# Kernel tuning notes

Hardware: AMD Instinct MI355X
Metric: run time of the kernel (lower is better)

## Reference

```python
import jax, jax.numpy as jnp
import numpy as np

B, S, E = 2, 2048, 1024
H = 16
D = E // H  # head_dim = 64
SCALE = D ** -0.5


def _rope_cos_sin(seq_len, dim, dtype=jnp.float32):
    inv_freq = 1.0 / (10000.0 ** (jnp.arange(0, dim, 2, dtype=jnp.float32) / dim))
    pos = jnp.arange(seq_len, dtype=jnp.float32)
    freqs = pos[:, None] * inv_freq[None, :]  # [S, D/2]
    return jnp.cos(freqs).astype(dtype), jnp.sin(freqs).astype(dtype)


def _apply_rope(x, cos, sin):
    # x: [B, H, S, D]; interleaved complex rotation on (even, odd) pairs
    x2 = x.reshape(*x.shape[:-1], D // 2, 2)
    xr, xi = x2[..., 0], x2[..., 1]
    c = cos[None, None, :, :]
    s = sin[None, None, :, :]
    out_r = xr * c - xi * s
    out_i = xr * s + xi * c
    return jnp.stack([out_r, out_i], axis=-1).reshape(x.shape)


def setup_inputs() -> dict:
    key = jax.random.key(0)
    k1, k2, k3, k4, k5 = jax.random.split(key, 5)
    query = jax.random.normal(k1, (B, S, E), dtype=jnp.float32)
    key_t = jax.random.normal(k2, (B, S, E), dtype=jnp.float32)
    value = jax.random.normal(k3, (B, S, E), dtype=jnp.float32)
    w_qkv = jax.random.normal(k4, (3 * E, E), dtype=jnp.float32) * 0.02
    w_out = jax.random.normal(k5, (E, E), dtype=jnp.float32) * 0.02
    return {"query": query, "key": key_t, "value": value,
            "w_qkv": w_qkv, "w_out": w_out}


def reference(query, key, value, w_qkv, w_out):
    # Fused QKV projection from query only (matches original module)
    qkv = jnp.einsum('bse,fe->bsf', query, w_qkv)  # [B, S, 3E]
    q, k, v = jnp.split(qkv, 3, axis=-1)
    to_heads = lambda t: t.reshape(B, S, H, D).transpose(0, 2, 1, 3)  # [B,H,S,D]
    q, k, v = to_heads(q), to_heads(k), to_heads(v)

    cos, sin = _rope_cos_sin(S, D, q.dtype)
    q = _apply_rope(q, cos, sin)
    k = _apply_rope(k, cos, sin)

    # Standard scaled dot-product attention (eval mode, no mask, no dropout)
    attn = jnp.einsum('bhsd,bhtd->bhst', q, k) * SCALE
    attn = jax.nn.softmax(attn.astype(jnp.float32), axis=-1).astype(q.dtype)
    ctx = jnp.einsum('bhst,bhtd->bhsd', attn, v)  # [B,H,S,D]

    out = ctx.transpose(0, 2, 1, 3).reshape(B, S, E)
    return jnp.einsum('bse,fe->bsf', out, w_out)
```

## Files before the change

### kernel.cpp

```cpp
#include <hip/hip_runtime.h>
#include <math.h>

typedef __attribute__((ext_vector_type(8))) __bf16 bf16x8;
typedef __attribute__((ext_vector_type(4))) __bf16 bf16x4;
typedef __attribute__((ext_vector_type(4))) float f32x4;

constexpr int kBATCH = 2;
constexpr int kS = 2048;
constexpr int kE = 1024;
constexpr int kH = 16;
constexpr int kD = 64;
constexpr float kScale = 0.125f;

__device__ inline void gl2lds16(const void* g, void* l) {
    __builtin_amdgcn_global_load_lds((const __attribute__((address_space(1))) void*)g,
                                     (__attribute__((address_space(3))) void*)l, 16, 0, 0);
}

__global__ __launch_bounds__(256) void cvt2_kernel(const float* __restrict__ a, __bf16* __restrict__ oa, int na,
                                                   const float* __restrict__ b, __bf16* __restrict__ ob) {
    int idx = (blockIdx.x * 256 + threadIdx.x) * 4;
    const float* src;
    __bf16* dst;
    if (idx < na) { src = a + idx; dst = oa + idx; }
    else          { src = b + (idx - na); dst = ob + (idx - na); }
    float4 f = *(const float4*)src;
    bf16x4 r;
    r[0] = (__bf16)f.x; r[1] = (__bf16)f.y; r[2] = (__bf16)f.z; r[3] = (__bf16)f.w;
    *(bf16x4*)dst = r;
}

template <int TN, typename TC>
__global__ __launch_bounds__(256) void gemm_bt_kernel(const __bf16* __restrict__ A,
                                                      const __bf16* __restrict__ W,
                                                      TC* __restrict__ C,
                                                      int M, int N, int K) {
    constexpr int NI = TN / 32;
    __shared__ __bf16 As[128 * 64] __attribute__((aligned(16)));
    __shared__ __bf16 Bs[TN * 64] __attribute__((aligned(16)));

    const int tid  = threadIdx.x;
    const int lane = tid & 63;
    const int quad = lane >> 4;
    const int l16  = lane & 15;
    const int rx   = l16 & 7;
    const int wave = tid >> 6;
    const int wm   = (wave >> 1) * 64;
    const int wn   = (wave & 1) * (TN / 2);
    const int m0   = blockIdx.y * 128;
    const int n0   = blockIdx.x * TN;

    const int srow8  = lane >> 3;
    const int schunk = ((lane & 7) ^ srow8) * 8;

    f32x4 zero = {0.f, 0.f, 0.f, 0.f};
    f32x4 acc[4][NI];
#pragma unroll
    for (int i = 0; i < 4; ++i)
#pragma unroll
        for (int j = 0; j < NI; ++j) acc[i][j] = zero;

    for (int kt = 0; kt < K; kt += 64) {
        __syncthreads();
#pragma unroll
        for (int i = 0; i < 4; ++i) {
            int rbase = wave * 32 + i * 8;
            gl2lds16(A + (size_t)(m0 + rbase + srow8) * K + kt + schunk, &As[rbase * 64]);
        }
#pragma unroll
        for (int i = 0; i < NI; ++i) {
            int rbase = wave * (TN / 4) + i * 8;
            gl2lds16(W + (size_t)(n0 + rbase + srow8) * K + kt + schunk, &Bs[rbase * 64]);
        }
        __syncthreads();

#pragma unroll
        for (int kk = 0; kk < 2; ++kk) {
            bf16x8 af[4], bf[NI];
#pragma unroll
            for (int mi = 0; mi < 4; ++mi)
                af[mi] = *(const bf16x8*)(&As[(wm + mi * 16 + l16) * 64 + (((kk * 4 + quad) ^ rx)) * 8]);
#pragma unroll
            for (int ni = 0; ni < NI; ++ni)
                bf[ni] = *(const bf16x8*)(&Bs[(wn + ni * 16 + l16) * 64 + (((kk * 4 + quad) ^ rx)) * 8]);
#pragma unroll
            for (int mi = 0; mi < 4; ++mi)
#pragma unroll
                for (int ni = 0; ni < NI; ++ni)
                    acc[mi][ni] = __builtin_amdgcn_mfma_f32_16x16x32_bf16(af[mi], bf[ni], acc[mi][ni], 0, 0, 0);
        }
    }

#pragma unroll
    for (int mi = 0; mi < 4; ++mi)
#pragma unroll
        for (int ni = 0; ni < NI; ++ni)
#pragma unroll
            for (int r = 0; r < 4; ++r) {
                int row = m0 + wm + mi * 16 + quad * 4 + r;
                int col = n0 + wn + ni * 16 + l16;
                C[(size_t)row * N + col] = (TC)acc[mi][ni][r];
            }
}

__global__ __launch_bounds__(256) void rope_vtrans_kernel(const __bf16* __restrict__ qkv,
                                                          __bf16* __restrict__ qd,
                                                          __bf16* __restrict__ kd,
                                                          __bf16* __restrict__ vt) {
    __shared__ __bf16 tile[64 * 72] __attribute__((aligned(16)));

    if (blockIdx.x < 8192) {
        int tid = blockIdx.x * 256 + threadIdx.x;
        int i = tid & 31;
        int h = (tid >> 5) & (kH - 1);
        int s = (tid >> 9) & (kS - 1);
        int b = tid >> 20;

        size_t rowbase = (size_t)(b * kS + s) * (3 * kE);
        int coff = h * kD + 2 * i;

        float qr = (float)qkv[rowbase + coff];
        float qi = (float)qkv[rowbase + coff + 1];
        float kr = (float)qkv[rowbase + kE + coff];
        float ki = (float)qkv[rowbase + kE + coff + 1];

        float inv = expf(-(float)i * (9.210340371976184f / 32.0f));
        float ang = (float)s * inv;
        float cv = cosf(ang);
        float sv = sinf(ang);

        size_t qbase = ((size_t)(b * kH + h) * kS + s) * kD + 2 * i;
        qd[qbase]     = (__bf16)(kScale * (qr * cv - qi * sv));
        qd[qbase + 1] = (__bf16)(kScale * (qr * sv + qi * cv));
        kd[qbase]     = (__bf16)(kr * cv - ki * sv);
        kd[qbase + 1] = (__bf16)(kr * sv + ki * cv);
    } else {
        int flat = blockIdx.x - 8192;
        int s0 = (flat & 31) * 64;
        int bh = flat >> 5;
        int b = bh >> 4, h = bh & 15;
        int tid = threadIdx.x;

#pragma unroll
        for (int p = 0; p < 2; ++p) {
            int c = tid + p * 256;
            int r = c >> 3, jc = c & 7;
            *(bf16x8*)&tile[r * 72 + jc * 8] =
                *(const bf16x8*)(qkv + (size_t)(b * kS + s0 + r) * (3 * kE) + 2 * kE + h * kD + jc * 8);
        }
        __syncthreads();
#pragma unroll
        for (int p = 0; p < 2; ++p) {
            int c = tid + p * 256;
            int d = c >> 3, jt = c & 7;
            bf16x8 v;
#pragma unroll
            for (int u = 0; u < 8; ++u) {
                int src = (jt >> 2) * 32 + ((u >> 2) << 4) + ((jt & 3) << 2) + (u & 3);
                v[u] = tile[src * 72 + d];
            }
            *(bf16x8*)(vt + (size_t)(bh * kD + d) * kS + s0 + jt * 8) = v;
        }
    }
}

__global__ __launch_bounds__(128) void attn_kernel(const __bf16* __restrict__ qd,
                                                   const __bf16* __restrict__ kd,
                                                   const __bf16* __restrict__ vt,
                                                   __bf16* __restrict__ ctx,
                                                   const float* __restrict__ wout,
                                                   __bf16* __restrict__ woutb) {
    __shared__ __bf16 Ks[2][64 * 64] __attribute__((aligned(16)));
    __shared__ __bf16 Vs[2][64 * 64] __attribute__((aligned(16)));

    const int lane = threadIdx.x & 63;
    const int wave = threadIdx.x >> 6;
    const int quad = lane >> 4;
    const int l16  = lane & 15;
    const int rx   = l16 & 7;

    {
        int base = blockIdx.x * 1024 + threadIdx.x * 8;
        float4 f0 = *(const float4*)(wout + base);
        float4 f1 = *(const float4*)(wout + base + 4);
        bf16x8 r;
        r[0] = (__bf16)f0.x; r[1] = (__bf16)f0.y; r[2] = (__bf16)f0.z; r[3] = (__bf16)f0.w;
        r[4] = (__bf16)f1.x; r[5] = (__bf16)f1.y; r[6] = (__bf16)f1.z; r[7] = (__bf16)f1.w;
        *(bf16x8*)(woutb + base) = r;
    }

    const int flat = blockIdx.x;
    const int s    = flat >> 3;
    const int bh   = (flat & 7) * 4 + (s >> 5);
    const int q0   = (s & 31) * 64;
    const int b  = bh >> 4;
    const int h  = bh & 15;

    const __bf16* qp = qd + (size_t)bh * kS * kD;
    const __bf16* kp = kd + (size_t)bh * kS * kD;
    const __bf16* vp = vt + (size_t)bh * kD * kS;

    const int srow8  = lane >> 3;
    const int schunk = ((lane & 7) ^ srow8) * 8;

    bf16x8 aq[2][2];
#pragma unroll
    for (int mi = 0; mi < 2; ++mi) {
        const __bf16* qrow = qp + (size_t)(q0 + wave * 32 + mi * 16 + l16) * kD + quad * 8;
        aq[mi][0] = *(const bf16x8*)(qrow);
        aq[mi][1] = *(const bf16x8*)(qrow + 32);
    }

    bf16x8 vone;
#pragma unroll
    for (int u = 0; u < 8; ++u) vone[u] = (__bf16)1.0f;

    f32x4 zero = {0.f, 0.f, 0.f, 0.f};
    f32x4 acc[2][4];
    f32x4 asum[2];
#pragma unroll
    for (int mi = 0; mi < 2; ++mi) {
        asum[mi] = zero;
#pragma unroll
        for (int i = 0; i < 4; ++i) acc[mi][i] = zero;
    }

#pragma unroll
    for (int c = 0; c < 4; ++c) {
        int i = wave * 4 + c;
        gl2lds16(kp + (size_t)(i * 8 + srow8) * kD + schunk, &Ks[0][i * 512]);
        gl2lds16(vp + (size_t)(i * 8 + srow8) * kS + schunk, &Vs[0][i * 512]);
    }

    const int nT = kS / 64;
    for (int it = 0; it < nT; ++it) {
        const int buf = it & 1;
        __syncthreads();
        if (it + 1 < nT) {
            int t1 = (it + 1) * 64;
#pragma unroll
            for (int c = 0; c < 4; ++c) {
                int i = wave * 4 + c;
                gl2lds16(kp + (size_t)(t1 + i * 8 + srow8) * kD + schunk, &Ks[buf ^ 1][i * 512]);
                gl2lds16(vp + (size_t)(i * 8 + srow8) * kS + t1 + schunk, &Vs[buf ^ 1][i * 512]);
            }
        }

#pragma unroll
        for (int ks = 0; ks < 2; ++ks) {
            bf16x8 ak[2][2];
#pragma unroll
            for (int t2 = 0; t2 < 2; ++t2) {
                int krow = (ks * 2 + t2) * 16 + l16;
                ak[t2][0] = *(const bf16x8*)&Ks[buf][krow * 64 + ((quad      ^ rx)) * 8];
                ak[t2][1] = *(const bf16x8*)&Ks[buf][krow * 64 + (((quad + 4) ^ rx)) * 8];
            }
            bf16x8 ap[2];
#pragma unroll
            for (int mi = 0; mi < 2; ++mi) {
                f32x4 s0 = __builtin_amdgcn_mfma_f32_16x16x32_bf16(ak[0][0], aq[mi][0], zero, 0, 0, 0);
                s0 = __builtin_amdgcn_mfma_f32_16x16x32_bf16(ak[0][1], aq[mi][1], s0, 0, 0, 0);
                f32x4 s1 = __builtin_amdgcn_mfma_f32_16x16x32_bf16(ak[1][0], aq[mi][0], zero, 0, 0, 0);
                s1 = __builtin_amdgcn_mfma_f32_16x16x32_bf16(ak[1][1], aq[mi][1], s1, 0, 0, 0);
                bf16x8 p;
                p[0] = (__bf16)__expf(s0[0]); p[1] = (__bf16)__expf(s0[1]);
                p[2] = (__bf16)__expf(s0[2]); p[3] = (__bf16)__expf(s0[3]);
                p[4] = (__bf16)__expf(s1[0]); p[5] = (__bf16)__expf(s1[1]);
                p[6] = (__bf16)__expf(s1[2]); p[7] = (__bf16)__expf(s1[3]);
                ap[mi] = p;
            }
#pragma unroll
            for (int mi = 0; mi < 2; ++mi)
                asum[mi] = __builtin_amdgcn_mfma_f32_16x16x32_bf16(ap[mi], vone, asum[mi], 0, 0, 0);
#pragma unroll
            for (int nt = 0; nt < 4; ++nt) {
                int drow = nt * 16 + l16;
                bf16x8 bv = *(const bf16x8*)&Vs[buf][drow * 64 + (((ks * 4 + quad) ^ rx)) * 8];
                acc[0][nt] = __builtin_amdgcn_mfma_f32_16x16x32_bf16(ap[0], bv, acc[0][nt], 0, 0, 0);
                acc[1][nt] = __builtin_amdgcn_mfma_f32_16x16x32_bf16(ap[1], bv, acc[1][nt], 0, 0, 0);
            }
        }
    }

#pragma unroll
    for (int mi = 0; mi < 2; ++mi)
#pragma unroll
        for (int r = 0; r < 4; ++r) {
            float inv_l = 1.0f / asum[mi][r];
            int srow_q = q0 + wave * 32 + mi * 16 + quad * 4 + r;
#pragma unroll
            for (int nt = 0; nt < 4; ++nt) {
                int col = h * kD + nt * 16 + l16;
                ctx[(size_t)(b * kS + srow_q) * kE + col] = (__bf16)(acc[mi][nt][r] * inv_l);
            }
        }
}

extern "C" void kernel_launch(void* const* d_in, const int* in_sizes, int n_in,
                              void* d_out, int out_size, void* d_ws, size_t ws_size,
                              hipStream_t stream) {
    const float* query = (const float*)d_in[0];
    const float* w_qkv = (const float*)d_in[3];
    const float* w_out = (const float*)d_in[4];
    float* out = (float*)d_out;

    const int M = kBATCH * kS;
    const int nQ = M * kE;
    const int nWqkv = 3 * kE * kE;

    char* ws = (char*)d_ws;
    __bf16* qkv_raw = (__bf16*)ws;
    __bf16* ctx     = (__bf16*)ws;
    __bf16* w_out_b = (__bf16*)(ws + (size_t)8388608);
    __bf16* qd      = (__bf16*)(ws + (size_t)25165824);
    __bf16* kd      = (__bf16*)(ws + (size_t)33554432);
    __bf16* vt      = (__bf16*)(ws + (size_t)41943040);
    __bf16* query_b = qd;
    __bf16* w_qkv_b = kd;

    cvt2_kernel<<<(nQ + nWqkv) / 1024, 256, 0, stream>>>(query, query_b, nQ, w_qkv, w_qkv_b);

    gemm_bt_kernel<128, __bf16>
        <<<dim3(3 * kE / 128, M / 128), 256, 0, stream>>>(query_b, w_qkv_b, qkv_raw, M, 3 * kE, kE);

    rope_vtrans_kernel<<<8192 + 1024, 256, 0, stream>>>(qkv_raw, qd, kd, vt);

    attn_kernel<<<1024, 128, 0, stream>>>(qd, kd, vt, ctx, w_out, w_out_b);

    gemm_bt_kernel<64, float>
        <<<dim3(kE / 64, M / 128), 256, 0, stream>>>(ctx, w_out_b, out, M, kE, kE);
}
```

Measured before the change: 226.7 us.

## Split attention KV range across waves and read K/V directly from global

Each block now runs four waves: two query halves times two key halves, each wave covering half the sequence. Partial sums and row sums are combined through shared memory at the end. The LDS double-buffered staging of K and V tiles is removed, so each wave loads its MFMA fragments straight from global memory and relies on the caches. This adds waves per block for more latency hiding, but loses LDS reuse and issues many small, strided global loads.

New measurement: 278.5 us. +22.8%, slower.

```diff
diff --git a/kernel.cpp b/kernel.cpp
--- a/kernel.cpp
+++ b/kernel.cpp
@@ -164,29 +164,27 @@
     }
 }
 
-__global__ __launch_bounds__(128) void attn_kernel(const __bf16* __restrict__ qd,
-                                                   const __bf16* __restrict__ kd,
-                                                   const __bf16* __restrict__ vt,
-                                                   __bf16* __restrict__ ctx,
-                                                   const float* __restrict__ wout,
-                                                   __bf16* __restrict__ woutb) {
-    __shared__ __bf16 Ks[2][64 * 64] __attribute__((aligned(16)));
-    __shared__ __bf16 Vs[2][64 * 64] __attribute__((aligned(16)));
-
-    const int lane = threadIdx.x & 63;
-    const int wave = threadIdx.x >> 6;
-    const int quad = lane >> 4;
-    const int l16  = lane & 15;
-    const int rx   = l16 & 7;
+__global__ __launch_bounds__(256, 4) void attn_kernel(const __bf16* __restrict__ qd,
+                                                      const __bf16* __restrict__ kd,
+                                                      const __bf16* __restrict__ vt,
+                                                      __bf16* __restrict__ ctx,
+                                                      const float* __restrict__ wout,
+                                                      __bf16* __restrict__ woutb) {
+    __shared__ float comb[2][64][40];
+
+    const int lane  = threadIdx.x & 63;
+    const int wave  = threadIdx.x >> 6;
+    const int qhalf = wave >> 1;
+    const int khalf = wave & 1;
+    const int quad  = lane >> 4;
+    const int l16   = lane & 15;
 
     {
-        int base = blockIdx.x * 1024 + threadIdx.x * 8;
-        float4 f0 = *(const float4*)(wout + base);
-        float4 f1 = *(const float4*)(wout + base + 4);
-        bf16x8 r;
-        r[0] = (__bf16)f0.x; r[1] = (__bf16)f0.y; r[2] = (__bf16)f0.z; r[3] = (__bf16)f0.w;
-        r[4] = (__bf16)f1.x; r[5] = (__bf16)f1.y; r[6] = (__bf16)f1.z; r[7] = (__bf16)f1.w;
-        *(bf16x8*)(woutb + base) = r;
+        int base = blockIdx.x * 1024 + threadIdx.x * 4;
+        float4 f = *(const float4*)(wout + base);
+        bf16x4 r;
+        r[0] = (__bf16)f.x; r[1] = (__bf16)f.y; r[2] = (__bf16)f.z; r[3] = (__bf16)f.w;
+        *(bf16x4*)(woutb + base) = r;
     }
 
     const int flat = blockIdx.x;
@@ -200,13 +198,10 @@
     const __bf16* kp = kd + (size_t)bh * kS * kD;
     const __bf16* vp = vt + (size_t)bh * kD * kS;
 
-    const int srow8  = lane >> 3;
-    const int schunk = ((lane & 7) ^ srow8) * 8;
-
     bf16x8 aq[2][2];
 #pragma unroll
     for (int mi = 0; mi < 2; ++mi) {
-        const __bf16* qrow = qp + (size_t)(q0 + wave * 32 + mi * 16 + l16) * kD + quad * 8;
+        const __bf16* qrow = qp + (size_t)(q0 + qhalf * 32 + mi * 16 + l16) * kD + quad * 8;
         aq[mi][0] = *(const bf16x8*)(qrow);
         aq[mi][1] = *(const bf16x8*)(qrow + 32);
     }
@@ -225,43 +220,27 @@
         for (int i = 0; i < 4; ++i) acc[mi][i] = zero;
     }
 
-#pragma unroll
-    for (int c = 0; c < 4; ++c) {
-        int i = wave * 4 + c;
-        gl2lds16(kp + (size_t)(i * 8 + srow8) * kD + schunk, &Ks[0][i * 512]);
-        gl2lds16(vp + (size_t)(i * 8 + srow8) * kS + schunk, &Vs[0][i * 512]);
-    }
-
-    const int nT = kS / 64;
-    for (int it = 0; it < nT; ++it) {
-        const int buf = it & 1;
-        __syncthreads();
-        if (it + 1 < nT) {
-            int t1 = (it + 1) * 64;
-#pragma unroll
-            for (int c = 0; c < 4; ++c) {
-                int i = wave * 4 + c;
-                gl2lds16(kp + (size_t)(t1 + i * 8 + srow8) * kD + schunk, &Ks[buf ^ 1][i * 512]);
-                gl2lds16(vp + (size_t)(i * 8 + srow8) * kS + t1 + schunk, &Vs[buf ^ 1][i * 512]);
-            }
-        }
-
+    const __bf16* kfrag = kp + (size_t)(khalf * 1024 + l16) * kD + quad * 8;
+    const __bf16* vfrag = vp + (size_t)l16 * kS + khalf * 1024 + quad * 8;
+
+#pragma unroll 2
+    for (int it = 0; it < 16; ++it) {
+        const __bf16* kt = kfrag + it * (64 * kD);
+        const __bf16* vtile = vfrag + it * 64;
 #pragma unroll
         for (int ks = 0; ks < 2; ++ks) {
-            bf16x8 ak[2][2];
-#pragma unroll
-            for (int t2 = 0; t2 < 2; ++t2) {
-                int krow = (ks * 2 + t2) * 16 + l16;
-                ak[t2][0] = *(const bf16x8*)&Ks[buf][krow * 64 + ((quad      ^ rx)) * 8];
-                ak[t2][1] = *(const bf16x8*)&Ks[buf][krow * 64 + (((quad + 4) ^ rx)) * 8];
-            }
+            const __bf16* kk = kt + ks * (32 * kD);
+            bf16x8 ak00 = *(const bf16x8*)(kk);
+            bf16x8 ak01 = *(const bf16x8*)(kk + 32);
+            bf16x8 ak10 = *(const bf16x8*)(kk + 16 * kD);
+            bf16x8 ak11 = *(const bf16x8*)(kk + 16 * kD + 32);
             bf16x8 ap[2];
 #pragma unroll
             for (int mi = 0; mi < 2; ++mi) {
-                f32x4 s0 = __builtin_amdgcn_mfma_f32_16x16x32_bf16(ak[0][0], aq[mi][0], zero, 0, 0, 0);
-                s0 = __builtin_amdgcn_mfma_f32_16x16x32_bf16(ak[0][1], aq[mi][1], s0, 0, 0, 0);
-                f32x4 s1 = __builtin_amdgcn_mfma_f32_16x16x32_bf16(ak[1][0], aq[mi][0], zero, 0, 0, 0);
-                s1 = __builtin_amdgcn_mfma_f32_16x16x32_bf16(ak[1][1], aq[mi][1], s1, 0, 0, 0);
+                f32x4 s0 = __builtin_amdgcn_mfma_f32_16x16x32_bf16(ak00, aq[mi][0], zero, 0, 0, 0);
+                s0 = __builtin_amdgcn_mfma_f32_16x16x32_bf16(ak01, aq[mi][1], s0, 0, 0, 0);
+                f32x4 s1 = __builtin_amdgcn_mfma_f32_16x16x32_bf16(ak10, aq[mi][0], zero, 0, 0, 0);
+                s1 = __builtin_amdgcn_mfma_f32_16x16x32_bf16(ak11, aq[mi][1], s1, 0, 0, 0);
                 bf16x8 p;
                 p[0] = (__bf16)__expf(s0[0]); p[1] = (__bf16)__expf(s0[1]);
                 p[2] = (__bf16)__expf(s0[2]); p[3] = (__bf16)__expf(s0[3]);
@@ -274,26 +253,39 @@
                 asum[mi] = __builtin_amdgcn_mfma_f32_16x16x32_bf16(ap[mi], vone, asum[mi], 0, 0, 0);
 #pragma unroll
             for (int nt = 0; nt < 4; ++nt) {
-                int drow = nt * 16 + l16;
-                bf16x8 bv = *(const bf16x8*)&Vs[buf][drow * 64 + (((ks * 4 + quad) ^ rx)) * 8];
+                bf16x8 bv = *(const bf16x8*)(vtile + (size_t)(nt * 16) * kS + ks * 32);
                 acc[0][nt] = __builtin_amdgcn_mfma_f32_16x16x32_bf16(ap[0], bv, acc[0][nt], 0, 0, 0);
                 acc[1][nt] = __builtin_amdgcn_mfma_f32_16x16x32_bf16(ap[1], bv, acc[1][nt], 0, 0, 0);
             }
         }
     }
 
-#pragma unroll
-    for (int mi = 0; mi < 2; ++mi)
-#pragma unroll
-        for (int r = 0; r < 4; ++r) {
-            float inv_l = 1.0f / asum[mi][r];
-            int srow_q = q0 + wave * 32 + mi * 16 + quad * 4 + r;
-#pragma unroll
-            for (int nt = 0; nt < 4; ++nt) {
-                int col = h * kD + nt * 16 + l16;
-                ctx[(size_t)(b * kS + srow_q) * kE + col] = (__bf16)(acc[mi][nt][r] * inv_l);
-            }
-        }
+    if (khalf) {
+#pragma unroll
+        for (int mi = 0; mi < 2; ++mi) {
+            *(f32x4*)&comb[qhalf][lane][mi * 20] = asum[mi];
+#pragma unroll
+            for (int nt = 0; nt < 4; ++nt)
+                *(f32x4*)&comb[qhalf][lane][mi * 20 + 4 + nt * 4] = acc[mi][nt];
+        }
+    }
+    __syncthreads();
+    if (!khalf) {
+#pragma unroll
+        for (int mi = 0; mi < 2; ++mi)
+#pragma unroll
+            for (int r = 0; r < 4; ++r) {
+                float l = asum[mi][r] + comb[qhalf][lane][mi * 20 + r];
+                float inv_l = 1.0f / l;
+                int srow_q = q0 + qhalf * 32 + mi * 16 + quad * 4 + r;
+#pragma unroll
+                for (int nt = 0; nt < 4; ++nt) {
+                    float o = acc[mi][nt][r] + comb[qhalf][lane][mi * 20 + 4 + nt * 4 + r];
+                    int col = h * kD + nt * 16 + l16;
+                    ctx[(size_t)(b * kS + srow_q) * kE + col] = (__bf16)(o * inv_l);
+                }
+            }
+    }
 }
 
 extern "C" void kernel_launch(void* const* d_in, const int* in_sizes, int n_in,
@@ -325,7 +317,7 @@
 
     rope_vtrans_kernel<<<8192 + 1024, 256, 0, stream>>>(qkv_raw, qd, kd, vt);
 
-    attn_kernel<<<1024, 128, 0, stream>>>(qd, kd, vt, ctx, w_out, w_out_b);
+    attn_kernel<<<1024, 256, 0, stream>>>(qd, kd, vt, ctx, w_out, w_out_b);
 
     gemm_bt_kernel<64, float>
         <<<dim3(kE / 64, M / 128), 256, 0, stream>>>(ctx, w_out_b, out, M, kE, kE);
```

## Split attention work across four waves with 16 query rows each

Applied to the files above, without the earlier changes.

Attention blocks go from 128 to 256 threads, and each wave now owns 16 query rows instead of 32. This halves the per-wave accumulator registers and raises the wave count per block. The K/V tile loads are spread over four waves, and the inner loop is restructured to compute all four score groups before the exp/PV step. The cost is less reuse of the K and V fragments read from LDS per wave, so LDS read traffic per FLOP doubles.

Measured after the change: 207.4 us. -8.5%, faster.

```diff
diff --git a/kernel.cpp b/kernel.cpp
--- a/kernel.cpp
+++ b/kernel.cpp
@@ -164,12 +164,12 @@
     }
 }
 
-__global__ __launch_bounds__(128) void attn_kernel(const __bf16* __restrict__ qd,
-                                                   const __bf16* __restrict__ kd,
-                                                   const __bf16* __restrict__ vt,
-                                                   __bf16* __restrict__ ctx,
-                                                   const float* __restrict__ wout,
-                                                   __bf16* __restrict__ woutb) {
+__global__ __launch_bounds__(256, 4) void attn_kernel(const __bf16* __restrict__ qd,
+                                                      const __bf16* __restrict__ kd,
+                                                      const __bf16* __restrict__ vt,
+                                                      __bf16* __restrict__ ctx,
+                                                      const float* __restrict__ wout,
+                                                      __bf16* __restrict__ woutb) {
     __shared__ __bf16 Ks[2][64 * 64] __attribute__((aligned(16)));
     __shared__ __bf16 Vs[2][64 * 64] __attribute__((aligned(16)));
 
@@ -180,13 +180,11 @@
     const int rx   = l16 & 7;
 
     {
-        int base = blockIdx.x * 1024 + threadIdx.x * 8;
-        float4 f0 = *(const float4*)(wout + base);
-        float4 f1 = *(const float4*)(wout + base + 4);
-        bf16x8 r;
-        r[0] = (__bf16)f0.x; r[1] = (__bf16)f0.y; r[2] = (__bf16)f0.z; r[3] = (__bf16)f0.w;
-        r[4] = (__bf16)f1.x; r[5] = (__bf16)f1.y; r[6] = (__bf16)f1.z; r[7] = (__bf16)f1.w;
-        *(bf16x8*)(woutb + base) = r;
+        int base = blockIdx.x * 1024 + threadIdx.x * 4;
+        float4 f = *(const float4*)(wout + base);
+        bf16x4 r;
+        r[0] = (__bf16)f.x; r[1] = (__bf16)f.y; r[2] = (__bf16)f.z; r[3] = (__bf16)f.w;
+        *(bf16x4*)(woutb + base) = r;
     }
 
     const int flat = blockIdx.x;
@@ -203,12 +201,11 @@
     const int srow8  = lane >> 3;
     const int schunk = ((lane & 7) ^ srow8) * 8;
 
-    bf16x8 aq[2][2];
-#pragma unroll
-    for (int mi = 0; mi < 2; ++mi) {
-        const __bf16* qrow = qp + (size_t)(q0 + wave * 32 + mi * 16 + l16) * kD + quad * 8;
-        aq[mi][0] = *(const bf16x8*)(qrow);
-        aq[mi][1] = *(const bf16x8*)(qrow + 32);
+    bf16x8 aq0, aq1;
+    {
+        const __bf16* qrow = qp + (size_t)(q0 + wave * 16 + l16) * kD + quad * 8;
+        aq0 = *(const bf16x8*)(qrow);
+        aq1 = *(const bf16x8*)(qrow + 32);
     }
 
     bf16x8 vone;
@@ -216,18 +213,14 @@
     for (int u = 0; u < 8; ++u) vone[u] = (__bf16)1.0f;
 
     f32x4 zero = {0.f, 0.f, 0.f, 0.f};
-    f32x4 acc[2][4];
-    f32x4 asum[2];
-#pragma unroll
-    for (int mi = 0; mi < 2; ++mi) {
-        asum[mi] = zero;
-#pragma unroll
-        for (int i = 0; i < 4; ++i) acc[mi][i] = zero;
-    }
-
-#pragma unroll
-    for (int c = 0; c < 4; ++c) {
-        int i = wave * 4 + c;
+    f32x4 acc[4];
+    f32x4 asum = zero;
+#pragma unroll
+    for (int i = 0; i < 4; ++i) acc[i] = zero;
+
+#pragma unroll
+    for (int c = 0; c < 2; ++c) {
+        int i = wave * 2 + c;
         gl2lds16(kp + (size_t)(i * 8 + srow8) * kD + schunk, &Ks[0][i * 512]);
         gl2lds16(vp + (size_t)(i * 8 + srow8) * kS + schunk, &Vs[0][i * 512]);
     }
@@ -239,61 +232,55 @@
         if (it + 1 < nT) {
             int t1 = (it + 1) * 64;
 #pragma unroll
-            for (int c = 0; c < 4; ++c) {
-                int i = wave * 4 + c;
+            for (int c = 0; c < 2; ++c) {
+                int i = wave * 2 + c;
                 gl2lds16(kp + (size_t)(t1 + i * 8 + srow8) * kD + schunk, &Ks[buf ^ 1][i * 512]);
                 gl2lds16(vp + (size_t)(i * 8 + srow8) * kS + t1 + schunk, &Vs[buf ^ 1][i * 512]);
             }
         }
 
-#pragma unroll
-        for (int ks = 0; ks < 2; ++ks) {
-            bf16x8 ak[2][2];
-#pragma unroll
-            for (int t2 = 0; t2 < 2; ++t2) {
-                int krow = (ks * 2 + t2) * 16 + l16;
-                ak[t2][0] = *(const bf16x8*)&Ks[buf][krow * 64 + ((quad      ^ rx)) * 8];
-                ak[t2][1] = *(const bf16x8*)&Ks[buf][krow * 64 + (((quad + 4) ^ rx)) * 8];
-            }
-            bf16x8 ap[2];
-#pragma unroll
-            for (int mi = 0; mi < 2; ++mi) {
-                f32x4 s0 = __builtin_amdgcn_mfma_f32_16x16x32_bf16(ak[0][0], aq[mi][0], zero, 0, 0, 0);
-                s0 = __builtin_amdgcn_mfma_f32_16x16x32_bf16(ak[0][1], aq[mi][1], s0, 0, 0, 0);
-                f32x4 s1 = __builtin_amdgcn_mfma_f32_16x16x32_bf16(ak[1][0], aq[mi][0], zero, 0, 0, 0);
-                s1 = __builtin_amdgcn_mfma_f32_16x16x32_bf16(ak[1][1], aq[mi][1], s1, 0, 0, 0);
-                bf16x8 p;
-                p[0] = (__bf16)__expf(s0[0]); p[1] = (__bf16)__expf(s0[1]);
-                p[2] = (__bf16)__expf(s0[2]); p[3] = (__bf16)__expf(s0[3]);
-                p[4] = (__bf16)__expf(s1[0]); p[5] = (__bf16)__expf(s1[1]);
-                p[6] = (__bf16)__expf(s1[2]); p[7] = (__bf16)__expf(s1[3]);
-                ap[mi] = p;
-            }
-#pragma unroll
-            for (int mi = 0; mi < 2; ++mi)
-                asum[mi] = __builtin_amdgcn_mfma_f32_16x16x32_bf16(ap[mi], vone, asum[mi], 0, 0, 0);
-#pragma unroll
-            for (int nt = 0; nt < 4; ++nt) {
-                int drow = nt * 16 + l16;
-                bf16x8 bv = *(const bf16x8*)&Vs[buf][drow * 64 + (((ks * 4 + quad) ^ rx)) * 8];
-                acc[0][nt] = __builtin_amdgcn_mfma_f32_16x16x32_bf16(ap[0], bv, acc[0][nt], 0, 0, 0);
-                acc[1][nt] = __builtin_amdgcn_mfma_f32_16x16x32_bf16(ap[1], bv, acc[1][nt], 0, 0, 0);
-            }
-        }
-    }
-
-#pragma unroll
-    for (int mi = 0; mi < 2; ++mi)
+        f32x4 sg[4];
+#pragma unroll
+        for (int g = 0; g < 4; ++g) {
+            int krow = g * 16 + l16;
+            bf16x8 a0 = *(const bf16x8*)&Ks[buf][krow * 64 + ((quad      ^ rx)) * 8];
+            bf16x8 a1 = *(const bf16x8*)&Ks[buf][krow * 64 + (((quad + 4) ^ rx)) * 8];
+            f32x4 t = __builtin_amdgcn_mfma_f32_16x16x32_bf16(a0, aq0, zero, 0, 0, 0);
+            sg[g] = __builtin_amdgcn_mfma_f32_16x16x32_bf16(a1, aq1, t, 0, 0, 0);
+        }
+
+        bf16x8 ap0, ap1;
 #pragma unroll
         for (int r = 0; r < 4; ++r) {
-            float inv_l = 1.0f / asum[mi][r];
-            int srow_q = q0 + wave * 32 + mi * 16 + quad * 4 + r;
-#pragma unroll
-            for (int nt = 0; nt < 4; ++nt) {
-                int col = h * kD + nt * 16 + l16;
-                ctx[(size_t)(b * kS + srow_q) * kE + col] = (__bf16)(acc[mi][nt][r] * inv_l);
-            }
-        }
+            ap0[r]     = (__bf16)__expf(sg[0][r]);
+            ap0[4 + r] = (__bf16)__expf(sg[1][r]);
+            ap1[r]     = (__bf16)__expf(sg[2][r]);
+            ap1[4 + r] = (__bf16)__expf(sg[3][r]);
+        }
+
+        asum = __builtin_amdgcn_mfma_f32_16x16x32_bf16(ap0, vone, asum, 0, 0, 0);
+        asum = __builtin_amdgcn_mfma_f32_16x16x32_bf16(ap1, vone, asum, 0, 0, 0);
+
+#pragma unroll
+        for (int nt = 0; nt < 4; ++nt) {
+            int drow = nt * 16 + l16;
+            bf16x8 bv0 = *(const bf16x8*)&Vs[buf][drow * 64 + ((quad      ^ (drow & 7))) * 8];
+            bf16x8 bv1 = *(const bf16x8*)&Vs[buf][drow * 64 + (((quad + 4) ^ (drow & 7))) * 8];
+            acc[nt] = __builtin_amdgcn_mfma_f32_16x16x32_bf16(ap0, bv0, acc[nt], 0, 0, 0);
+            acc[nt] = __builtin_amdgcn_mfma_f32_16x16x32_bf16(ap1, bv1, acc[nt], 0, 0, 0);
+        }
+    }
+
+#pragma unroll
+    for (int r = 0; r < 4; ++r) {
+        float inv_l = 1.0f / asum[r];
+        int srow_q = q0 + wave * 16 + quad * 4 + r;
+#pragma unroll
+        for (int nt = 0; nt < 4; ++nt) {
+            int col = h * kD + nt * 16 + l16;
+            ctx[(size_t)(b * kS + srow_q) * kE + col] = (__bf16)(acc[nt][r] * inv_l);
+        }
+    }
 }
 
 extern "C" void kernel_launch(void* const* d_in, const int* in_sizes, int n_in,
@@ -325,7 +312,7 @@
 
     rope_vtrans_kernel<<<8192 + 1024, 256, 0, stream>>>(qkv_raw, qd, kd, vt);
 
-    attn_kernel<<<1024, 128, 0, stream>>>(qd, kd, vt, ctx, w_out, w_out_b);
+    attn_kernel<<<1024, 256, 0, stream>>>(qd, kd, vt, ctx, w_out, w_out_b);
 
     gemm_bt_kernel<64, float>
         <<<dim3(kE / 64, M / 128), 256, 0, stream>>>(ctx, w_out_b, out, M, kE, kE);
```
